# Performance work log

Measured on AMD Instinct MI355X. Metric: run time of the kernel, lower is better.

Reference implementation:

```python
import jax, jax.numpy as jnp
import numpy as np

D_MODEL = 1024
HIDDEN = 2048
D_STATE = 16
KERN = 3
BATCH = 2
SEQ = 2048


def _layernorm(x, g, b, eps=1e-5):
    m = jnp.mean(x, axis=-1, keepdims=True)
    v = jnp.var(x, axis=-1, keepdims=True)
    return (x - m) * jax.lax.rsqrt(v + eps) * g + b


def setup_inputs() -> dict:
    key = jax.random.key(0)
    ks = jax.random.split(key, 10)
    w_scale = 0.02  # keep pre-activations in a sane range (mimics trained-net init)
    return {
        "x": jax.random.normal(ks[0], (BATCH, SEQ, D_MODEL), jnp.float32),
        "W_x": jax.random.normal(ks[1], (HIDDEN, D_MODEL), jnp.float32) * w_scale,
        "b_x": jnp.zeros((HIDDEN,), jnp.float32),
        "W_g": jax.random.normal(ks[2], (HIDDEN, D_MODEL), jnp.float32) * w_scale,
        "b_g": jnp.zeros((HIDDEN,), jnp.float32),
        "conv_w": jax.random.normal(ks[3], (HIDDEN, 1, KERN), jnp.float32) * 0.3,
        "conv_b": jnp.zeros((HIDDEN,), jnp.float32),
        "A_raw": jax.random.normal(ks[4], (HIDDEN, D_STATE), jnp.float32),
        "B_ssm": jax.random.normal(ks[5], (HIDDEN, D_STATE), jnp.float32),
        "C_ssm": jax.random.normal(ks[6], (HIDDEN, D_STATE), jnp.float32),
        "W_dt": jax.random.normal(ks[7], (HIDDEN, D_MODEL), jnp.float32) * w_scale,
        "b_dt": jnp.zeros((HIDDEN,), jnp.float32),
        "W_out": jax.random.normal(ks[8], (D_MODEL, HIDDEN), jnp.float32) * w_scale,
        "b_out": jnp.zeros((D_MODEL,), jnp.float32),
        "ln_g": jnp.ones((D_MODEL,), jnp.float32),
        "ln_b": jnp.zeros((D_MODEL,), jnp.float32),
    }


def reference(x, W_x, b_x, W_g, b_g, conv_w, conv_b, A_raw, B_ssm, C_ssm,
              W_dt, b_dt, W_out, b_out, ln_g, ln_b):
    # projections: u, gate
    u = jnp.einsum('bld,hd->blh', x, W_x) + b_x                    # [B,L,H]
    g = jax.nn.sigmoid(jnp.einsum('bld,hd->blh', x, W_g) + b_g)    # [B,L,H]
    # depthwise conv over time (padding = kernel//2, 'same' for odd kernel)
    pad = conv_w.shape[-1] // 2
    h = jax.lax.conv_general_dilated(
        jnp.transpose(u, (0, 2, 1)), conv_w,
        window_strides=(1,), padding=[(pad, pad)],
        feature_group_count=conv_w.shape[0],
        dimension_numbers=('NCH', 'OIH', 'NCH')) + conv_b[None, :, None]
    h = jnp.transpose(h, (0, 2, 1))                                # [B,L,H]
    u = u * g + h * (1.0 - g)
    # time-invariant dt per channel (mean over batch & time, clamped)
    dt = jax.nn.softplus(jnp.einsum('bld,hd->blh', x, W_dt) + b_dt).mean(axis=(0, 1))
    dt = jnp.clip(dt, 1e-3, 2.0)                                   # [H]
    # discretize
    A = -jax.nn.softplus(A_raw)                                    # [H,S]
    A_d = jnp.exp(A * dt[:, None])                                 # [H,S]
    B_d = (A_d - 1.0) / (A + 1e-6) * B_ssm                         # [H,S]
    # selective scan: state s[b,h,k] = A_d*s + B_d*u_t ; y = <s, C>
    Bsz, L, H = u.shape
    S = A_d.shape[1]

    def step(carry, u_t):                                          # u_t: [B,H]
        new = A_d[None] * carry + B_d[None] * u_t[:, :, None]      # [B,H,S]
        y_t = jnp.einsum('bhs,hs->bh', new, C_ssm)
        return new, y_t

    init = jnp.zeros((Bsz, H, S), dtype=u.dtype)
    _, ys = jax.lax.scan(step, init, jnp.transpose(u, (1, 0, 2)))  # ys: [L,B,H]
    y = jnp.transpose(ys, (1, 0, 2))                               # [B,L,H]
    out = jnp.einsum('blh,dh->bld', y, W_out) + b_out
    return _layernorm(x + out, ln_g, ln_b)
```

## Files before the change

kernel.cpp:

```cpp
#include <hip/hip_runtime.h>
#include <math.h>

#define D_MODEL 1024
#define HIDDEN  2048
#define D_STATE 16
#define BATCH   2
#define SEQ     2048
#define NTOK    (BATCH*SEQ)
#define CHUNK   32
#define NCHUNK  (SEQ/CHUNK)

typedef __attribute__((ext_vector_type(8))) short bf16x8;
typedef __attribute__((ext_vector_type(8))) unsigned short ushort8;
typedef __attribute__((ext_vector_type(4))) float f32x4;

#define GLOAD_LDS16(gptr, lptr) \
    __builtin_amdgcn_global_load_lds((const __attribute__((address_space(1))) void*)(gptr), \
                                     (__attribute__((address_space(3))) void*)(lptr), 16, 0, 0)

__device__ __forceinline__ float softplus_f(float x) {
    return fmaxf(x, 0.0f) + log1pf(expf(-fabsf(x)));
}
__device__ __forceinline__ float sigmoid_f(float x) {
    return 1.0f / (1.0f + expf(-x));
}
__device__ __forceinline__ ushort f2bf(float f) {
    unsigned u = __float_as_uint(f);
    unsigned r = (u + 0x7fffu + ((u >> 16) & 1u)) >> 16;
    return (ushort)r;
}
__device__ __forceinline__ float bf2f(ushort u) {
    return __uint_as_float(((unsigned)u) << 16);
}

__global__ __launch_bounds__(256) void cvt_all(
    const float* __restrict__ x, const float* __restrict__ Wx,
    const float* __restrict__ Wg, const float* __restrict__ Wdt,
    const float* __restrict__ Wout, ushort* __restrict__ arena)
{
    int i = blockIdx.x * 256 + threadIdx.x;
    const float* src; int base;
    if      (i < 1048576) { src = x;    base = 0; }
    else if (i < 1572864) { src = Wx;   base = 1048576; }
    else if (i < 2097152) { src = Wg;   base = 1572864; }
    else if (i < 2621440) { src = Wdt;  base = 2097152; }
    else                  { src = Wout; base = 2621440; }
    float4 v = reinterpret_cast<const float4*>(src)[i - base];
    ushort4 o = { f2bf(v.x), f2bf(v.y), f2bf(v.z), f2bf(v.w) };
    reinterpret_cast<ushort4*>(arena)[i] = o;
}

__device__ __forceinline__ void kloop_pipe3(
    const ushort* __restrict__ A, const ushort* __restrict__ B,
    int K, int m0, int n0, ushort* As, ushort* Bs,
    f32x4 (&acc)[4][4], int lane, int w, int wm, int wn)
{
    const int lr   = lane >> 2;
    const int qsrc = (lane & 3) ^ ((lane >> 3) & 3);
    const int kc   = qsrc * 8;
    const int quad = lane >> 4;
    const int fr   = lane & 15;
    const int chq  = quad ^ ((fr >> 1) & 3);

    const int slab0 = w * 2;
    const int r0 = slab0 * 16 + lr;
    const int r1 = r0 + 16;
    const size_t ga0 = (size_t)(m0 + r0) * K + kc;
    const size_t ga1 = (size_t)(m0 + r1) * K + kc;
    const size_t gb0 = (size_t)(n0 + r0) * K + kc;
    const size_t gb1 = (size_t)(n0 + r1) * K + kc;

    const int niter = K / 32;
    GLOAD_LDS16(A + ga0,      &As[slab0 * 512]);
    GLOAD_LDS16(A + ga1,      &As[slab0 * 512 + 512]);
    GLOAD_LDS16(B + gb0,      &Bs[slab0 * 512]);
    GLOAD_LDS16(B + gb1,      &Bs[slab0 * 512 + 512]);
    GLOAD_LDS16(A + ga0 + 32, &As[4096 + slab0 * 512]);
    GLOAD_LDS16(A + ga1 + 32, &As[4096 + slab0 * 512 + 512]);
    GLOAD_LDS16(B + gb0 + 32, &Bs[4096 + slab0 * 512]);
    GLOAD_LDS16(B + gb1 + 32, &Bs[4096 + slab0 * 512 + 512]);

    int buf = 0;
    for (int i = 0; i < niter; i++) {
        asm volatile("s_waitcnt vmcnt(4) lgkmcnt(0)" ::: "memory");
        asm volatile("s_barrier" ::: "memory");
        int nb = buf + 2; if (nb >= 3) nb -= 3;
        const size_t koff = (i + 2 < niter) ? (size_t)(i + 2) * 32 : 0;
        GLOAD_LDS16(A + ga0 + koff, &As[nb * 4096 + slab0 * 512]);
        GLOAD_LDS16(A + ga1 + koff, &As[nb * 4096 + slab0 * 512 + 512]);
        GLOAD_LDS16(B + gb0 + koff, &Bs[nb * 4096 + slab0 * 512]);
        GLOAD_LDS16(B + gb1 + koff, &Bs[nb * 4096 + slab0 * 512 + 512]);

        const ushort* as = &As[buf * 4096];
        const ushort* bs = &Bs[buf * 4096];
        bf16x8 af[4], bfv[4];
        #pragma unroll
        for (int t = 0; t < 4; t++) {
            af[t]  = *reinterpret_cast<const bf16x8*>(&as[(wm * 64 + t * 16 + fr) * 32 + chq * 8]);
            bfv[t] = *reinterpret_cast<const bf16x8*>(&bs[(wn * 64 + t * 16 + fr) * 32 + chq * 8]);
        }
        #pragma unroll
        for (int ii = 0; ii < 4; ii++)
            #pragma unroll
            for (int jj = 0; jj < 4; jj++)
                acc[ii][jj] = __builtin_amdgcn_mfma_f32_16x16x32_bf16(af[ii], bfv[jj], acc[ii][jj], 0, 0, 0);
        buf = (buf == 2) ? 0 : buf + 1;
    }
    asm volatile("s_waitcnt vmcnt(0) lgkmcnt(0)" ::: "memory");
    asm volatile("s_barrier" ::: "memory");
}

__global__ __launch_bounds__(256) void proj_gemm_fused(
    const ushort* __restrict__ xbf, const ushort* __restrict__ Wcat,
    const float* __restrict__ b_x, const float* __restrict__ b_g,
    const float* __restrict__ b_dt, ushort* __restrict__ u_out,
    ushort* __restrict__ g_out, float* __restrict__ dt_sum)
{
    __shared__ ushort S[24576];
    ushort* As = S;
    ushort* Bs = S + 12288;
    const int tid = threadIdx.x, lane = tid & 63, w = tid >> 6;
    const int wm = w & 1, wn = w >> 1;
    const int m0 = blockIdx.x * 128, n0 = blockIdx.y * 128;
    const int quad = lane >> 4, fr = lane & 15;

    f32x4 acc[4][4];
    #pragma unroll
    for (int i = 0; i < 4; i++)
        #pragma unroll
        for (int j = 0; j < 4; j++)
            acc[i][j] = (f32x4){0.f, 0.f, 0.f, 0.f};

    kloop_pipe3(xbf, Wcat, D_MODEL, m0, n0, As, Bs, acc, lane, w, wm, wn);

    const int region = n0 >> 11;
    const int ncb = n0 & 2047;

    if (region == 2) {
        #pragma unroll
        for (int j = 0; j < 4; j++) {
            int n = ncb + wn * 64 + j * 16 + fr;
            float bj = b_dt[n];
            float s = 0.f;
            #pragma unroll
            for (int i = 0; i < 4; i++)
                #pragma unroll
                for (int r = 0; r < 4; r++)
                    s += softplus_f(acc[i][j][r] + bj);
            s += __shfl_xor(s, 16);
            s += __shfl_xor(s, 32);
            if (lane < 16) atomicAdd(&dt_sum[n], s);
        }
    } else {
        const float* bias = region ? b_g : b_x;
        ushort* out = region ? g_out : u_out;
        ushort* Cs = S;
        #pragma unroll
        for (int j = 0; j < 4; j++) {
            int col = wn * 64 + j * 16 + fr;
            float bj = bias[ncb + col];
            #pragma unroll
            for (int i = 0; i < 4; i++) {
                int row = wm * 64 + i * 16 + quad * 4;
                #pragma unroll
                for (int r = 0; r < 4; r++) {
                    float v = acc[i][j][r] + bj;
                    if (region) v = sigmoid_f(v);
                    Cs[(row + r) * 128 + col] = f2bf(v);
                }
            }
        }
        __syncthreads();
        #pragma unroll
        for (int k = 0; k < 8; k++) {
            int v = k * 256 + tid;
            int row = v >> 4, c = (v & 15) * 8;
            *reinterpret_cast<ushort8*>(&out[(size_t)(m0 + row) * HIDDEN + ncb + c]) =
                *reinterpret_cast<const ushort8*>(&Cs[v * 8]);
        }
    }
}

__global__ __launch_bounds__(256) void gemm_out64(
    const ushort* __restrict__ ybf, const ushort* __restrict__ Wout,
    const float* __restrict__ b_out, const float* __restrict__ x,
    float* __restrict__ resid)
{
    __shared__ ushort S[36864];
    ushort* As = S;
    ushort* Bs = S + 12288;
    const int tid = threadIdx.x, lane = tid & 63, w = tid >> 6;
    const int m0 = blockIdx.x * 64, n0 = blockIdx.y * 128;
    const int quad = lane >> 4, fr = lane & 15;
    const int lr8  = lane >> 3;
    const int q8   = (lane & 7) ^ (lr8 & 7);
    const int K = HIDDEN;

    const size_t ga = (size_t)(m0 + w * 16 + lr8) * K + q8 * 8;
    const size_t gb = (size_t)(n0 + w * 32 + lr8) * K + q8 * 8;

    f32x4 acc[4][2];
    #pragma unroll
    for (int i = 0; i < 4; i++)
        #pragma unroll
        for (int j = 0; j < 2; j++)
            acc[i][j] = (f32x4){0.f, 0.f, 0.f, 0.f};

#define STAGE_OUT(KT, BUF) do {                                                   \
    const size_t ko_ = (size_t)(KT) * 64;                                         \
    GLOAD_LDS16(ybf  + ga + ko_,            &As[(BUF)*4096 + (w*2+0)*512]);       \
    GLOAD_LDS16(ybf  + ga + 8*K + ko_,      &As[(BUF)*4096 + (w*2+1)*512]);       \
    GLOAD_LDS16(Wout + gb + ko_,            &Bs[(BUF)*8192 + (w*4+0)*512]);       \
    GLOAD_LDS16(Wout + gb + 8*K + ko_,      &Bs[(BUF)*8192 + (w*4+1)*512]);       \
    GLOAD_LDS16(Wout + gb + 16*K + ko_,     &Bs[(BUF)*8192 + (w*4+2)*512]);       \
    GLOAD_LDS16(Wout + gb + 24*K + ko_,     &Bs[(BUF)*8192 + (w*4+3)*512]);       \
  } while (0)

    STAGE_OUT(0, 0);
    STAGE_OUT(1, 1);

    int buf = 0;
    for (int t = 0; t < 32; t++) {
        asm volatile("s_waitcnt vmcnt(6) lgkmcnt(0)" ::: "memory");
        asm volatile("s_barrier" ::: "memory");
        int nb = buf + 2; if (nb >= 3) nb -= 3;
        const int kt = (t + 2 < 32) ? (t + 2) : 0;
        STAGE_OUT(kt, nb);

        const ushort* as = &As[buf * 4096];
        const ushort* bs = &Bs[buf * 8192];
        #pragma unroll
        for (int ks = 0; ks < 2; ks++) {
            const int ch = ((ks * 4 + quad) ^ (fr & 7)) * 8;
            bf16x8 af[4], bfv[2];
            #pragma unroll
            for (int mi = 0; mi < 4; mi++)
                af[mi] = *reinterpret_cast<const bf16x8*>(&as[(mi * 16 + fr) * 64 + ch]);
            #pragma unroll
            for (int nj = 0; nj < 2; nj++)
                bfv[nj] = *reinterpret_cast<const bf16x8*>(&bs[(w * 32 + nj * 16 + fr) * 64 + ch]);
            #pragma unroll
            for (int mi = 0; mi < 4; mi++)
                #pragma unroll
                for (int nj = 0; nj < 2; nj++)
                    acc[mi][nj] = __builtin_amdgcn_mfma_f32_16x16x32_bf16(af[mi], bfv[nj], acc[mi][nj], 0, 0, 0);
        }
        buf = (buf == 2) ? 0 : buf + 1;
    }
    asm volatile("s_waitcnt vmcnt(0) lgkmcnt(0)" ::: "memory");
    asm volatile("s_barrier" ::: "memory");
#undef STAGE_OUT

    float* Sf = (float*)S;
    #pragma unroll
    for (int nj = 0; nj < 2; nj++) {
        int col = w * 32 + nj * 16 + fr;
        float bj = b_out[n0 + col];
        #pragma unroll
        for (int mi = 0; mi < 4; mi++) {
            int row = mi * 16 + quad * 4;
            #pragma unroll
            for (int r = 0; r < 4; r++)
                Sf[(row + r) * 128 + col] = acc[mi][nj][r] + bj;
        }
    }
    __syncthreads();
    #pragma unroll
    for (int k = 0; k < 8; k++) {
        int v = k * 256 + tid;
        int row = v >> 5, c = (v & 31) * 4;
        size_t off = (size_t)(m0 + row) * D_MODEL + n0 + c;
        float4 xa = *reinterpret_cast<const float4*>(&x[off]);
        float4 cv = *reinterpret_cast<const float4*>(&Sf[v * 4]);
        float4 o = { cv.x + xa.x, cv.y + xa.y, cv.z + xa.z, cv.w + xa.w };
        *reinterpret_cast<float4*>(&resid[off]) = o;
    }
}

__global__ __launch_bounds__(256) void dt_finalize(
    const float* __restrict__ dt_sum, const float* __restrict__ A_raw,
    const float* __restrict__ B_ssm, float* __restrict__ A_d,
    float* __restrict__ B_d, float* __restrict__ A_dL)
{
    int i = blockIdx.x * 256 + threadIdx.x;
    if (i >= HIDDEN * D_STATE) return;
    int h = i >> 4;
    float dt = dt_sum[h] * (1.0f / NTOK);
    dt = fminf(fmaxf(dt, 1e-3f), 2.0f);
    float Av = -softplus_f(A_raw[i]);
    float Ad = expf(Av * dt);
    float Bd = (Ad - 1.0f) / (Av + 1e-6f) * B_ssm[i];
    A_d[i] = Ad;
    B_d[i] = Bd;
    A_dL[i] = expf(Av * dt * CHUNK);
}

__global__ __launch_bounds__(256) void scan_pass1(
    const ushort* __restrict__ u_bf, const ushort* __restrict__ g_bf,
    const float* __restrict__ conv_w, const float* __restrict__ conv_b,
    const float* __restrict__ A_d, const float* __restrict__ B_d,
    const float* __restrict__ C_ssm,
    ushort* __restrict__ ypart, float* __restrict__ states)
{
    int idx = blockIdx.x * 256 + threadIdx.x;
    int h  = idx & (HIDDEN - 1);
    int bc = idx >> 11;
    int c  = bc & (NCHUNK - 1);
    int b  = bc / NCHUNK;
    float Ad[D_STATE], Bd[D_STATE], Cv[D_STATE], st[D_STATE];
    const float4* a4 = reinterpret_cast<const float4*>(A_d  + h * D_STATE);
    const float4* b4 = reinterpret_cast<const float4*>(B_d  + h * D_STATE);
    const float4* c4 = reinterpret_cast<const float4*>(C_ssm + h * D_STATE);
    #pragma unroll
    for (int q = 0; q < 4; q++) {
        float4 av = a4[q], bv = b4[q], cv = c4[q];
        Ad[q*4+0]=av.x; Ad[q*4+1]=av.y; Ad[q*4+2]=av.z; Ad[q*4+3]=av.w;
        Bd[q*4+0]=bv.x; Bd[q*4+1]=bv.y; Bd[q*4+2]=bv.z; Bd[q*4+3]=bv.w;
        Cv[q*4+0]=cv.x; Cv[q*4+1]=cv.y; Cv[q*4+2]=cv.z; Cv[q*4+3]=cv.w;
    }
    #pragma unroll
    for (int s = 0; s < D_STATE; s++) st[s] = 0.f;

    float w0 = conv_w[h * 3 + 0], w1 = conv_w[h * 3 + 1];
    float w2 = conv_w[h * 3 + 2], cb = conv_b[h];
    const int tok0 = c * CHUNK;
    const size_t base = ((size_t)b * SEQ + tok0) * HIDDEN + h;
    float u_prev = (tok0 > 0) ? bf2f(u_bf[base - HIDDEN]) : 0.f;
    float u_cur  = bf2f(u_bf[base]);
    for (int l = 0; l < CHUNK; l++) {
        float u_next = (tok0 + l + 1 < SEQ) ? bf2f(u_bf[base + (size_t)(l + 1) * HIDDEN]) : 0.f;
        float gv = bf2f(g_bf[base + (size_t)l * HIDDEN]);
        float conv = u_prev * w0 + u_cur * w1 + u_next * w2 + cb;
        float uv = u_cur * gv + conv * (1.0f - gv);
        float y0 = 0.f, y1 = 0.f, y2 = 0.f, y3 = 0.f;
        #pragma unroll
        for (int s = 0; s < D_STATE; s += 4) {
            st[s+0] = fmaf(Ad[s+0], st[s+0], Bd[s+0] * uv);
            st[s+1] = fmaf(Ad[s+1], st[s+1], Bd[s+1] * uv);
            st[s+2] = fmaf(Ad[s+2], st[s+2], Bd[s+2] * uv);
            st[s+3] = fmaf(Ad[s+3], st[s+3], Bd[s+3] * uv);
            y0 = fmaf(st[s+0], Cv[s+0], y0);
            y1 = fmaf(st[s+1], Cv[s+1], y1);
            y2 = fmaf(st[s+2], Cv[s+2], y2);
            y3 = fmaf(st[s+3], Cv[s+3], y3);
        }
        ypart[base + (size_t)l * HIDDEN] = f2bf((y0 + y1) + (y2 + y3));
        u_prev = u_cur; u_cur = u_next;
    }
    float4* sp = reinterpret_cast<float4*>(states + ((size_t)bc * HIDDEN + h) * D_STATE);
    #pragma unroll
    for (int q = 0; q < 4; q++)
        sp[q] = (float4){st[q*4+0], st[q*4+1], st[q*4+2], st[q*4+3]};
}

__global__ __launch_bounds__(256) void scan_pass2(
    float* __restrict__ states, const float* __restrict__ A_dL)
{
    int idx = blockIdx.x * 256 + threadIdx.x;
    int s = idx & 15;
    int h = (idx >> 4) & (HIDDEN - 1);
    int b = idx >> 15;
    float aL = A_dL[h * D_STATE + s];
    float carry = 0.f;
    for (int c = 0; c < NCHUNK; c++) {
        size_t addr = (((size_t)(b * NCHUNK + c) * HIDDEN) + h) * D_STATE + s;
        float fin = states[addr];
        states[addr] = carry;
        carry = fmaf(aL, carry, fin);
    }
}

__global__ __launch_bounds__(256) void scan_pass3(
    const ushort* __restrict__ ypart, const float* __restrict__ states,
    const float* __restrict__ A_d, const float* __restrict__ C_ssm,
    ushort* __restrict__ ybf)
{
    int idx = blockIdx.x * 256 + threadIdx.x;
    int h  = idx & (HIDDEN - 1);
    int bc = idx >> 11;
    int c  = bc & (NCHUNK - 1);
    int b  = bc / NCHUNK;
    float Ad[D_STATE], t[D_STATE];
    const float* sp = states + ((size_t)bc * HIDDEN + h) * D_STATE;
    #pragma unroll
    for (int s = 0; s < D_STATE; s++) {
        float a = A_d[h * D_STATE + s];
        Ad[s] = a;
        t[s] = C_ssm[h * D_STATE + s] * a * sp[s];
    }
    const size_t base = ((size_t)b * SEQ + (size_t)c * CHUNK) * HIDDEN + h;
    for (int l = 0; l < CHUNK; l++) {
        float c0 = 0.f, c1 = 0.f;
        #pragma unroll
        for (int s = 0; s < D_STATE; s += 2) {
            c0 += t[s];
            c1 += t[s + 1];
            t[s] *= Ad[s];
            t[s + 1] *= Ad[s + 1];
        }
        ybf[base + (size_t)l * HIDDEN] = f2bf(bf2f(ypart[base + (size_t)l * HIDDEN]) + (c0 + c1));
    }
}

__global__ __launch_bounds__(256) void ln_kernel(
    const float* __restrict__ resid, const float* __restrict__ ln_g,
    const float* __restrict__ ln_b, float* __restrict__ out)
{
    int row = blockIdx.x;
    int tid = threadIdx.x;
    const float4 v = reinterpret_cast<const float4*>(resid + (size_t)row * D_MODEL)[tid];
    float s  = v.x + v.y + v.z + v.w;
    float ss = v.x * v.x + v.y * v.y + v.z * v.z + v.w * v.w;
    #pragma unroll
    for (int off = 32; off > 0; off >>= 1) {
        s  += __shfl_down(s, off);
        ss += __shfl_down(ss, off);
    }
    __shared__ float sbuf[4], ssbuf[4];
    int wid = tid >> 6, lane = tid & 63;
    if (lane == 0) { sbuf[wid] = s; ssbuf[wid] = ss; }
    __syncthreads();
    float tot  = sbuf[0] + sbuf[1] + sbuf[2] + sbuf[3];
    float tot2 = ssbuf[0] + ssbuf[1] + ssbuf[2] + ssbuf[3];
    float mean = tot * (1.0f / D_MODEL);
    float var  = tot2 * (1.0f / D_MODEL) - mean * mean;
    float rstd = rsqrtf(var + 1e-5f);
    const float4 gv = reinterpret_cast<const float4*>(ln_g)[tid];
    const float4 bv = reinterpret_cast<const float4*>(ln_b)[tid];
    float4 o;
    o.x = (v.x - mean) * rstd * gv.x + bv.x;
    o.y = (v.y - mean) * rstd * gv.y + bv.y;
    o.z = (v.z - mean) * rstd * gv.z + bv.z;
    o.w = (v.w - mean) * rstd * gv.w + bv.w;
    reinterpret_cast<float4*>(out + (size_t)row * D_MODEL)[tid] = o;
}

extern "C" void kernel_launch(void* const* d_in, const int* in_sizes, int n_in,
                              void* d_out, int out_size, void* d_ws, size_t ws_size,
                              hipStream_t stream) {
    const float* x      = (const float*)d_in[0];
    const float* W_x    = (const float*)d_in[1];
    const float* b_x    = (const float*)d_in[2];
    const float* W_g    = (const float*)d_in[3];
    const float* b_g    = (const float*)d_in[4];
    const float* conv_w = (const float*)d_in[5];
    const float* conv_b = (const float*)d_in[6];
    const float* A_raw  = (const float*)d_in[7];
    const float* B_ssm  = (const float*)d_in[8];
    const float* C_ssm  = (const float*)d_in[9];
    const float* W_dt   = (const float*)d_in[10];
    const float* b_dt   = (const float*)d_in[11];
    const float* W_out  = (const float*)d_in[12];
    const float* b_out  = (const float*)d_in[13];
    const float* ln_g   = (const float*)d_in[14];
    const float* ln_b   = (const float*)d_in[15];

    char* W = (char*)d_ws;
    ushort* arena   = (ushort*)(W);
    ushort* x_bf    = arena;
    ushort* Wcat    = arena + 4194304;
    ushort* Wout_bf = arena + 10485760;
    ushort* u_bf    = (ushort*)(W + (24ull << 20));
    ushort* g_bf    = (ushort*)(W + (40ull << 20));
    ushort* ypart   = (ushort*)(W + (56ull << 20));
    float*  resid   = (float*)(W + (40ull << 20));
    float*  states  = (float*)(W);
    float*  dt_sum  = (float*)(W + (80ull << 20));
    float*  A_d     = (float*)(W + (80ull << 20) + 65536);
    float*  B_d     = (float*)(W + (80ull << 20) + 65536 + 131072);
    float*  A_dL    = (float*)(W + (80ull << 20) + 65536 + 262144);
    ushort* y_bf    = u_bf;

    hipMemsetAsync(dt_sum, 0, HIDDEN * sizeof(float), stream);

    dim3 blk(256);
    cvt_all<<<12288, blk, 0, stream>>>(x, W_x, W_g, W_dt, W_out, arena);

    dim3 grid_proj(NTOK / 128, 3 * HIDDEN / 128);
    proj_gemm_fused<<<grid_proj, blk, 0, stream>>>(x_bf, Wcat, b_x, b_g, b_dt,
                                                   u_bf, g_bf, dt_sum);
    dt_finalize<<<(HIDDEN * D_STATE) / 256, blk, 0, stream>>>(dt_sum, A_raw, B_ssm,
                                                              A_d, B_d, A_dL);
    scan_pass1<<<(BATCH * NCHUNK * HIDDEN) / 256, blk, 0, stream>>>(
        u_bf, g_bf, conv_w, conv_b, A_d, B_d, C_ssm, ypart, states);
    scan_pass2<<<(BATCH * HIDDEN * D_STATE) / 256, blk, 0, stream>>>(states, A_dL);
    scan_pass3<<<(BATCH * NCHUNK * HIDDEN) / 256, blk, 0, stream>>>(ypart, states, A_d,
                                                                    C_ssm, y_bf);
    dim3 grid_out(NTOK / 64, D_MODEL / 128);
    gemm_out64<<<grid_out, blk, 0, stream>>>(y_bf, Wout_bf, b_out, x, resid);
    ln_kernel<<<NTOK, blk, 0, stream>>>(resid, ln_g, ln_b, (float*)d_out);
}
```

Baseline: 288.2 us.

## Replace triple-buffered projection GEMM loop with single-buffer loop; batch scan_pass2 loads

Removes the 3-stage global-to-LDS prefetch pipeline in the projection GEMM and replaces it with a single-buffered loop that loads one K-slice, waits on all outstanding loads, computes, and then barriers. This shrinks shared memory from 48KB to 32KB, which may let more blocks share a CU, but gives up the overlap of loads with MFMA work. Separately, scan_pass2 now issues eight chunk-state loads ahead of their serial carry updates, to hide memory latency in the sequential combine. An extra __syncthreads is added before the epilogue reuses shared memory.

```diff
diff --git a/kernel.cpp b/kernel.cpp
--- a/kernel.cpp
+++ b/kernel.cpp
@@ -50,79 +50,28 @@
     reinterpret_cast<ushort4*>(arena)[i] = o;
 }
 
-__device__ __forceinline__ void kloop_pipe3(
-    const ushort* __restrict__ A, const ushort* __restrict__ B,
-    int K, int m0, int n0, ushort* As, ushort* Bs,
-    f32x4 (&acc)[4][4], int lane, int w, int wm, int wn)
-{
-    const int lr   = lane >> 2;
-    const int qsrc = (lane & 3) ^ ((lane >> 3) & 3);
-    const int kc   = qsrc * 8;
-    const int quad = lane >> 4;
-    const int fr   = lane & 15;
-    const int chq  = quad ^ ((fr >> 1) & 3);
-
-    const int slab0 = w * 2;
-    const int r0 = slab0 * 16 + lr;
-    const int r1 = r0 + 16;
-    const size_t ga0 = (size_t)(m0 + r0) * K + kc;
-    const size_t ga1 = (size_t)(m0 + r1) * K + kc;
-    const size_t gb0 = (size_t)(n0 + r0) * K + kc;
-    const size_t gb1 = (size_t)(n0 + r1) * K + kc;
-
-    const int niter = K / 32;
-    GLOAD_LDS16(A + ga0,      &As[slab0 * 512]);
-    GLOAD_LDS16(A + ga1,      &As[slab0 * 512 + 512]);
-    GLOAD_LDS16(B + gb0,      &Bs[slab0 * 512]);
-    GLOAD_LDS16(B + gb1,      &Bs[slab0 * 512 + 512]);
-    GLOAD_LDS16(A + ga0 + 32, &As[4096 + slab0 * 512]);
-    GLOAD_LDS16(A + ga1 + 32, &As[4096 + slab0 * 512 + 512]);
-    GLOAD_LDS16(B + gb0 + 32, &Bs[4096 + slab0 * 512]);
-    GLOAD_LDS16(B + gb1 + 32, &Bs[4096 + slab0 * 512 + 512]);
-
-    int buf = 0;
-    for (int i = 0; i < niter; i++) {
-        asm volatile("s_waitcnt vmcnt(4) lgkmcnt(0)" ::: "memory");
-        asm volatile("s_barrier" ::: "memory");
-        int nb = buf + 2; if (nb >= 3) nb -= 3;
-        const size_t koff = (i + 2 < niter) ? (size_t)(i + 2) * 32 : 0;
-        GLOAD_LDS16(A + ga0 + koff, &As[nb * 4096 + slab0 * 512]);
-        GLOAD_LDS16(A + ga1 + koff, &As[nb * 4096 + slab0 * 512 + 512]);
-        GLOAD_LDS16(B + gb0 + koff, &Bs[nb * 4096 + slab0 * 512]);
-        GLOAD_LDS16(B + gb1 + koff, &Bs[nb * 4096 + slab0 * 512 + 512]);
-
-        const ushort* as = &As[buf * 4096];
-        const ushort* bs = &Bs[buf * 4096];
-        bf16x8 af[4], bfv[4];
-        #pragma unroll
-        for (int t = 0; t < 4; t++) {
-            af[t]  = *reinterpret_cast<const bf16x8*>(&as[(wm * 64 + t * 16 + fr) * 32 + chq * 8]);
-            bfv[t] = *reinterpret_cast<const bf16x8*>(&bs[(wn * 64 + t * 16 + fr) * 32 + chq * 8]);
-        }
-        #pragma unroll
-        for (int ii = 0; ii < 4; ii++)
-            #pragma unroll
-            for (int jj = 0; jj < 4; jj++)
-                acc[ii][jj] = __builtin_amdgcn_mfma_f32_16x16x32_bf16(af[ii], bfv[jj], acc[ii][jj], 0, 0, 0);
-        buf = (buf == 2) ? 0 : buf + 1;
-    }
-    asm volatile("s_waitcnt vmcnt(0) lgkmcnt(0)" ::: "memory");
-    asm volatile("s_barrier" ::: "memory");
-}
-
 __global__ __launch_bounds__(256) void proj_gemm_fused(
     const ushort* __restrict__ xbf, const ushort* __restrict__ Wcat,
     const float* __restrict__ b_x, const float* __restrict__ b_g,
     const float* __restrict__ b_dt, ushort* __restrict__ u_out,
     ushort* __restrict__ g_out, float* __restrict__ dt_sum)
 {
-    __shared__ ushort S[24576];
+    __shared__ ushort S[16384];
     ushort* As = S;
-    ushort* Bs = S + 12288;
+    ushort* Bs = S + 4096;
     const int tid = threadIdx.x, lane = tid & 63, w = tid >> 6;
     const int wm = w & 1, wn = w >> 1;
     const int m0 = blockIdx.x * 128, n0 = blockIdx.y * 128;
     const int quad = lane >> 4, fr = lane & 15;
+    const int lr   = lane >> 2;
+    const int qsrc = (lane & 3) ^ ((lane >> 3) & 3);
+    const int chq  = quad ^ ((fr >> 1) & 3);
+    const int K = D_MODEL;
+
+    const size_t ga0 = (size_t)(m0 + w * 16 + lr) * K + qsrc * 8;
+    const size_t ga1 = ga0 + (size_t)64 * K;
+    const size_t gb0 = (size_t)(n0 + w * 16 + lr) * K + qsrc * 8;
+    const size_t gb1 = gb0 + (size_t)64 * K;
 
     f32x4 acc[4][4];
     #pragma unroll
@@ -131,7 +80,28 @@
         for (int j = 0; j < 4; j++)
             acc[i][j] = (f32x4){0.f, 0.f, 0.f, 0.f};
 
-    kloop_pipe3(xbf, Wcat, D_MODEL, m0, n0, As, Bs, acc, lane, w, wm, wn);
+    for (int t = 0; t < K / 32; t++) {
+        const size_t koff = (size_t)t * 32;
+        GLOAD_LDS16(xbf  + ga0 + koff, &As[w * 512]);
+        GLOAD_LDS16(xbf  + ga1 + koff, &As[2048 + w * 512]);
+        GLOAD_LDS16(Wcat + gb0 + koff, &Bs[w * 512]);
+        GLOAD_LDS16(Wcat + gb1 + koff, &Bs[2048 + w * 512]);
+        asm volatile("s_waitcnt vmcnt(0) lgkmcnt(0)" ::: "memory");
+        asm volatile("s_barrier" ::: "memory");
+
+        bf16x8 af[4], bfv[4];
+        #pragma unroll
+        for (int q = 0; q < 4; q++) {
+            af[q]  = *reinterpret_cast<const bf16x8*>(&As[(wm * 64 + q * 16 + fr) * 32 + chq * 8]);
+            bfv[q] = *reinterpret_cast<const bf16x8*>(&Bs[(wn * 64 + q * 16 + fr) * 32 + chq * 8]);
+        }
+        #pragma unroll
+        for (int ii = 0; ii < 4; ii++)
+            #pragma unroll
+            for (int jj = 0; jj < 4; jj++)
+                acc[ii][jj] = __builtin_amdgcn_mfma_f32_16x16x32_bf16(af[ii], bfv[jj], acc[ii][jj], 0, 0, 0);
+        asm volatile("s_barrier" ::: "memory");
+    }
 
     const int region = n0 >> 11;
     const int ncb = n0 & 2047;
@@ -155,6 +125,7 @@
         const float* bias = region ? b_g : b_x;
         ushort* out = region ? g_out : u_out;
         ushort* Cs = S;
+        __syncthreads();
         #pragma unroll
         for (int j = 0; j < 4; j++) {
             int col = wn * 64 + j * 16 + fr;
@@ -362,11 +333,19 @@
     int b = idx >> 15;
     float aL = A_dL[h * D_STATE + s];
     float carry = 0.f;
-    for (int c = 0; c < NCHUNK; c++) {
-        size_t addr = (((size_t)(b * NCHUNK + c) * HIDDEN) + h) * D_STATE + s;
-        float fin = states[addr];
-        states[addr] = carry;
-        carry = fmaf(aL, carry, fin);
+    const size_t cstride = (size_t)HIDDEN * D_STATE;
+    float* p = states + ((size_t)b * NCHUNK * HIDDEN + h) * D_STATE + s;
+    #pragma unroll 1
+    for (int cb = 0; cb < NCHUNK / 8; cb++) {
+        float fin[8];
+        #pragma unroll
+        for (int j = 0; j < 8; j++) fin[j] = p[(size_t)j * cstride];
+        #pragma unroll
+        for (int j = 0; j < 8; j++) {
+            p[(size_t)j * cstride] = carry;
+            carry = fmaf(aL, carry, fin[j]);
+        }
+        p += 8 * cstride;
     }
 }
 
```

Result: slower. 306.3 us (+6.3%).
